# Performance work log

Hardware: AMD Instinct MI355X
Metric: run time of the kernel (lower is better)

The kernel has to match this reference:

```python
import jax, jax.numpy as jnp
import numpy as np

EMB = 2048
HEADS = 16


def setup_inputs() -> dict:
    key = jax.random.key(0)
    k_x, k_wqkv, k_bqkv, k_wo, k_bo = jax.random.split(key, 5)
    B, S, E = 2, 2048, EMB
    x = jax.random.normal(k_x, (B, S, E), dtype=jnp.float32)
    # nn.Linear weights stored as (in, out) for x @ W + b convention
    W_qkv = jax.random.normal(k_wqkv, (E, 3 * E), dtype=jnp.float32) * 0.02
    b_qkv = jax.random.normal(k_bqkv, (3 * E,), dtype=jnp.float32) * 0.02
    W_out = jax.random.normal(k_wo, (E, E), dtype=jnp.float32) * 0.02
    b_out = jax.random.normal(k_bo, (E,), dtype=jnp.float32) * 0.02
    return {"x": x, "W_qkv": W_qkv, "b_qkv": b_qkv, "W_out": W_out, "b_out": b_out}


def reference(x, W_qkv, b_qkv, W_out, b_out):
    B, S, E = x.shape
    H = HEADS
    dh = E // H
    # QKV projection: (B,S,3E)
    qkv = x @ W_qkv + b_qkv
    # Faithful to torch: reshape (B,S,H,3*dh) THEN split -> interleaved per-head q/k/v
    qkv = qkv.reshape(B, S, H, 3 * dh).transpose(0, 2, 1, 3)  # (B,H,S,3*dh)
    q, k, v = jnp.split(qkv, 3, axis=-1)  # each (B,H,S,dh)
    q = q / jnp.asarray(dh, q.dtype) ** 0.5
    scores = jnp.einsum('bhqd,bhkd->bhqk', q, k)  # (B,H,S,S)
    weights = jax.nn.softmax(scores, axis=-1)
    attn = jnp.einsum('bhqk,bhkd->bhqd', weights, v)  # (B,H,S,dh)
    attn = attn.transpose(0, 2, 1, 3).reshape(B, S, E)
    return attn @ W_out + b_out
```

## Files before the change

kernel.cpp:

```cpp
#include <hip/hip_runtime.h>
#include <type_traits>
#include <utility>

#define DI __device__ __forceinline__

typedef unsigned short u16;
typedef float f32x4 __attribute__((ext_vector_type(4)));
typedef float f32x16 __attribute__((ext_vector_type(16)));
typedef short s16x8 __attribute__((ext_vector_type(8)));
typedef __bf16 bf16x8 __attribute__((ext_vector_type(8)));

template <typename V, typename = void>
struct mfma_ok : std::false_type {};
template <typename V>
struct mfma_ok<V, std::void_t<decltype(__builtin_amdgcn_mfma_f32_16x16x32_bf16(
    std::declval<V>(), std::declval<V>(), std::declval<f32x4>(), 0, 0, 0))>>
    : std::true_type {};
using frag_t = std::conditional_t<mfma_ok<bf16x8>::value, bf16x8, s16x8>;

union U128 {
  int4 i;
  frag_t f;
  u16 s[8];
};

DI f32x4 mfma16(const U128& a, const U128& b, f32x4 c) {
  return __builtin_amdgcn_mfma_f32_16x16x32_bf16(a.f, b.f, c, 0, 0, 0);
}
DI f32x16 mfma32(const U128& a, const U128& b, f32x16 c) {
  return __builtin_amdgcn_mfma_f32_32x32x16_bf16(a.f, b.f, c, 0, 0, 0);
}

DI u16 f2b(float x) {
  union { float f; unsigned u; } v; v.f = x;
  unsigned r = v.u + 0x7FFFu + ((v.u >> 16) & 1u);
  return (u16)(r >> 16);
}

DI unsigned pk2bf(float a, float b) {
  unsigned short ua = __builtin_bit_cast(unsigned short, (__bf16)a);
  unsigned short ub = __builtin_bit_cast(unsigned short, (__bf16)b);
  return (unsigned)ua | ((unsigned)ub << 16);
}

#if __has_builtin(__builtin_amdgcn_exp2f)
#define EXP2F __builtin_amdgcn_exp2f
#else
#define EXP2F exp2f
#endif

DI void plswap(unsigned& lo, unsigned& hi) {
  asm("v_permlane32_swap_b32 %0, %1" : "+v"(lo), "+v"(hi));
}

typedef __attribute__((address_space(1))) void gas_t;
typedef __attribute__((address_space(3))) void las_t;
DI void gll16(const void* g, void* l) {
  __builtin_amdgcn_global_load_lds((gas_t*)g, (las_t*)l, 16, 0, 0);
}

#define QSCALE 0.12751791437603762f

__global__ __launch_bounds__(256) void k_conv_bf16(const float* __restrict__ in,
                                                   u16* __restrict__ out, int n4) {
  int i = blockIdx.x * 256 + threadIdx.x;
  if (i >= n4) return;
  float4 v = ((const float4*)in)[i];
  ushort4 o;
  o.x = f2b(v.x); o.y = f2b(v.y); o.z = f2b(v.z); o.w = f2b(v.w);
  ((ushort4*)out)[i] = o;
}

__global__ __launch_bounds__(256) void k_transpose_f2b(const float* __restrict__ in,
                                                       u16* __restrict__ out,
                                                       int R, int C) {
  __shared__ __attribute__((aligned(16))) u16 Tb[64][68];
  int t = threadIdx.x;
  long r0 = (long)blockIdx.y * 64, c0 = (long)blockIdx.x * 64;
  int cq = (t & 15) * 4, rr = t >> 4;
#pragma unroll
  for (int it = 0; it < 4; ++it) {
    int r = rr + it * 16;
    float4 v = *(const float4*)(in + (r0 + r) * C + c0 + cq);
    Tb[r][cq + 0] = f2b(v.x); Tb[r][cq + 1] = f2b(v.y);
    Tb[r][cq + 2] = f2b(v.z); Tb[r][cq + 3] = f2b(v.w);
  }
  __syncthreads();
#pragma unroll
  for (int it = 0; it < 2; ++it) {
    int ci = it * 256 + t;
    int cc = ci >> 3, ch = ci & 7, rb = ch * 8;
    unsigned p0 = Tb[rb + 0][cc] | ((unsigned)Tb[rb + 1][cc] << 16);
    unsigned p1 = Tb[rb + 2][cc] | ((unsigned)Tb[rb + 3][cc] << 16);
    unsigned p2 = Tb[rb + 4][cc] | ((unsigned)Tb[rb + 5][cc] << 16);
    unsigned p3 = Tb[rb + 6][cc] | ((unsigned)Tb[rb + 7][cc] << 16);
    *(int4*)(out + (c0 + cc) * R + r0 + rb) = make_int4(p0, p1, p2, p3);
  }
}

template <int MODE>
__global__ __launch_bounds__(256, 4) void k_gemm_bt(const u16* __restrict__ A,
                                                    const u16* __restrict__ Bt,
                                                    const float* __restrict__ bias,
                                                    void* __restrict__ Cout,
                                                    u16* __restrict__ qb,
                                                    u16* __restrict__ kbv,
                                                    u16* __restrict__ vb,
                                                    int n_off,
                                                    int M, int N, int K) {
  __shared__ __attribute__((aligned(16))) u16 As[128 * 64];
  __shared__ __attribute__((aligned(16))) u16 Bs[128 * 64];
  int t = threadIdx.x;
  int lane = t & 63, w = t >> 6, quad = lane >> 4, l15 = lane & 15;
  long m0 = (long)blockIdx.y * 128, n0 = n_off + (long)blockIdx.x * 128;
  int wr = (w >> 1) * 64, wc = (w & 1) * 64;
  int sw = l15 & 7;
  f32x4 acc[4][4] = {};
  for (int k0 = 0; k0 < K; k0 += 64) {
    __syncthreads();
#pragma unroll
    for (int it = 0; it < 4; ++it) {
      int ci = it * 256 + t;
      int row = ci >> 3, cl = (ci & 7) ^ (row & 7);
      gll16(A + (m0 + row) * K + k0 + cl * 8, As + ci * 8);
      gll16(Bt + (n0 + row) * K + k0 + cl * 8, Bs + ci * 8);
    }
    __syncthreads();
#pragma unroll
    for (int kk = 0; kk < 2; ++kk) {
      U128 a[4], b[4];
#pragma unroll
      for (int i = 0; i < 4; ++i)
        a[i].i = *(const int4*)(As + (wr + i * 16 + l15) * 64 + (((kk * 4 + quad) ^ sw) << 3));
#pragma unroll
      for (int j = 0; j < 4; ++j)
        b[j].i = *(const int4*)(Bs + (wc + j * 16 + l15) * 64 + (((kk * 4 + quad) ^ sw) << 3));
#pragma unroll
      for (int i = 0; i < 4; ++i)
#pragma unroll
        for (int j = 0; j < 4; ++j)
          acc[i][j] = mfma16(a[i], b[j], acc[i][j]);
    }
  }
  float bj[4];
#pragma unroll
  for (int j = 0; j < 4; ++j) bj[j] = bias[n0 + wc + j * 16 + l15];

  int hidx = (int)(n0 / 384);
  int rsel = (int)(n0 - hidx * 384) >> 7;
  u16* route = (MODE == 1) ? (rsel == 0 ? qb : rsel == 1 ? kbv : vb) : nullptr;

#pragma unroll
  for (int i = 0; i < 4; ++i) {
#pragma unroll
    for (int rr2 = 0; rr2 < 4; ++rr2) {
      long row = m0 + wr + i * 16 + quad * 4 + rr2;
#pragma unroll
      for (int j = 0; j < 4; ++j) {
        float v = acc[i][j][rr2] + bj[j];
        if (MODE == 1) {
          if (rsel == 0) v *= QSCALE;
          int bidx = (int)(row >> 11), s = (int)(row & 2047);
          long obase = ((long)(bidx * 16 + hidx) * 2048 + s) * 128;
          int dh = wc + j * 16 + l15;
          unsigned pb = f2b(v);
          unsigned other = __shfl_xor(pb, 1);
          if (!(l15 & 1))
            ((unsigned*)route)[(obase + dh) >> 1] = pb | (other << 16);
        } else {
          long col = n0 + wc + j * 16 + l15;
          unsigned bits = __float_as_uint(v);
          unsigned other = __shfl_xor(bits, 1);
          if (!(l15 & 1)) {
            uint2 pr; pr.x = bits; pr.y = other;
            *(uint2*)((float*)Cout + row * N + col) = pr;
          }
        }
      }
    }
  }
}

__global__ __launch_bounds__(256) void k_extract_vt(const u16* __restrict__ vb,
                                                    u16* __restrict__ vt) {
  __shared__ __attribute__((aligned(16))) u16 Vb[64][136];
  int t = threadIdx.x;
  int s0 = blockIdx.x * 64;
  int bh = blockIdx.y;
  long inbase = ((long)bh * 2048 + s0) * 128;
#pragma unroll
  for (int it = 0; it < 4; ++it) {
    int ci = it * 256 + t;
    int s = ci >> 4, ch = ci & 15;
    int4 v = *(const int4*)(vb + inbase + s * 128 + ch * 8);
    *(int4*)(&Vb[s][ch * 8]) = v;
  }
  __syncthreads();
  long outbase = (long)bh * 128 * 2048 + s0;
#pragma unroll
  for (int it = 0; it < 4; ++it) {
    int ci = it * 256 + t;
    int d = ci >> 3, ch = ci & 7, sb = ch * 8;
    unsigned p0 = Vb[sb + 0][d] | ((unsigned)Vb[sb + 1][d] << 16);
    unsigned p1 = Vb[sb + 2][d] | ((unsigned)Vb[sb + 3][d] << 16);
    unsigned p2 = Vb[sb + 4][d] | ((unsigned)Vb[sb + 5][d] << 16);
    unsigned p3 = Vb[sb + 6][d] | ((unsigned)Vb[sb + 7][d] << 16);
    *(int4*)(vt + outbase + (long)d * 2048 + sb) = make_int4(p0, p1, p2, p3);
  }
}

__global__ __launch_bounds__(256, 2) void k_flash(const u16* __restrict__ qb,
                                                  const u16* __restrict__ kb,
                                                  const u16* __restrict__ vt,
                                                  u16* __restrict__ attn) {
  __shared__ __attribute__((aligned(16))) u16 Ks[2][64 * 128];
  __shared__ __attribute__((aligned(16))) u16 Vts[2][128 * 64];
  int t = threadIdx.x;
  int lane = t & 63, w = t >> 6, l31 = lane & 31, h = lane >> 5;
  int q0 = blockIdx.x * 128 + w * 32;
  int bh = blockIdx.y, b = bh >> 4, hd = bh & 15;

  const u16* qbase = qb + ((long)bh * 2048 + q0 + l31) * 128;
  U128 qf[8];
#pragma unroll
  for (int dht = 0; dht < 8; ++dht)
    qf[dht].i = *(const int4*)(qbase + dht * 16 + h * 8);
  __syncthreads();

  f32x16 O[4] = {};
  float ls0 = 0.f, ls1 = 0.f, ls2 = 0.f, ls3 = 0.f;
  const u16* kbh = kb + (long)bh * 2048 * 128;
  long vbase = (long)bh * 128 * 2048;

  unsigned swx = (unsigned)(((l31 & 7) << 3) ^ (h << 3));
  unsigned kinv = ((unsigned)l31 << 7) ^ swx;
  unsigned vinv = ((unsigned)l31 << 6) ^ swx;

  auto stage = [&](int buf, int k0) {
#pragma unroll
    for (int it = 0; it < 4; ++it) {
      int ci = it * 256 + t;
      int key = ci >> 4, cp = ci & 15, cl = cp ^ (key & 7);
      gll16(kbh + (long)(k0 + key) * 128 + cl * 8, &Ks[buf][0] + ci * 8);
    }
#pragma unroll
    for (int it = 0; it < 4; ++it) {
      int ci = it * 256 + t;
      int d = ci >> 3, cp = ci & 7, cl = cp ^ (d & 7);
      gll16(vt + vbase + (long)d * 2048 + k0 + cl * 8, &Vts[buf][0] + ci * 8);
    }
  };

  stage(0, 0);
  int cur = 0;
  for (int k0 = 0; k0 < 2048; k0 += 64) {
    if (k0 + 64 < 2048) {
      stage(cur ^ 1, k0 + 64);
      asm volatile("s_waitcnt vmcnt(8)" ::: "memory");
    } else {
      asm volatile("s_waitcnt vmcnt(0)" ::: "memory");
    }
    __builtin_amdgcn_s_barrier();
    asm volatile("" ::: "memory");
    const u16* KbT = &Ks[cur][0];
    const u16* VbT = &Vts[cur][0];

    f32x16 St0 = {}, St1 = {};
    __builtin_amdgcn_s_setprio(1);
#pragma unroll
    for (int dht = 0; dht < 8; ++dht) {
      U128 kf;
      kf.i = *(const int4*)(KbT + (kinv ^ (unsigned)(dht << 4)));
      St0 = mfma32(kf, qf[dht], St0);
    }
#pragma unroll
    for (int dht = 0; dht < 8; ++dht) {
      U128 kf;
      kf.i = *(const int4*)(KbT + (kinv ^ (unsigned)(dht << 4)) + 4096);
      St1 = mfma32(kf, qf[dht], St1);
    }
    __builtin_amdgcn_s_setprio(0);

    auto pv = [&](int kt, const U128& pfk) {
#pragma unroll
      for (int dht = 0; dht < 4; ++dht) {
        U128 vf;
        vf.i = *(const int4*)(VbT + (vinv ^ (unsigned)(kt << 4)) + dht * 2048);
        O[dht] = mfma32(vf, pfk, O[dht]);
      }
    };
    auto mkpf = [&](const float* p) {
      unsigned w0 = pk2bf(p[0], p[1]);
      unsigned w1 = pk2bf(p[2], p[3]);
      unsigned w2 = pk2bf(p[4], p[5]);
      unsigned w3 = pk2bf(p[6], p[7]);
      plswap(w0, w2);
      plswap(w1, w3);
      U128 r; r.i = make_int4(w0, w1, w2, w3);
      return r;
    };

    float p0[16];
#pragma unroll
    for (int r = 0; r < 16; r += 4) {
      p0[r + 0] = EXP2F(St0[r + 0]); ls0 += p0[r + 0];
      p0[r + 1] = EXP2F(St0[r + 1]); ls1 += p0[r + 1];
      p0[r + 2] = EXP2F(St0[r + 2]); ls2 += p0[r + 2];
      p0[r + 3] = EXP2F(St0[r + 3]); ls3 += p0[r + 3];
    }
    U128 pf0 = mkpf(&p0[0]);
    U128 pf1 = mkpf(&p0[8]);

    pv(0, pf0);

    float p1[16];
#pragma unroll
    for (int r = 0; r < 8; r += 4) {
      p1[r + 0] = EXP2F(St1[r + 0]); ls0 += p1[r + 0];
      p1[r + 1] = EXP2F(St1[r + 1]); ls1 += p1[r + 1];
      p1[r + 2] = EXP2F(St1[r + 2]); ls2 += p1[r + 2];
      p1[r + 3] = EXP2F(St1[r + 3]); ls3 += p1[r + 3];
    }
    pv(1, pf1);

#pragma unroll
    for (int r = 8; r < 16; r += 4) {
      p1[r + 0] = EXP2F(St1[r + 0]); ls0 += p1[r + 0];
      p1[r + 1] = EXP2F(St1[r + 1]); ls1 += p1[r + 1];
      p1[r + 2] = EXP2F(St1[r + 2]); ls2 += p1[r + 2];
      p1[r + 3] = EXP2F(St1[r + 3]); ls3 += p1[r + 3];
    }
    U128 pf2 = mkpf(&p1[0]);
    U128 pf3 = mkpf(&p1[8]);

    __builtin_amdgcn_s_setprio(1);
    pv(2, pf2);
    pv(3, pf3);
    __builtin_amdgcn_s_setprio(0);

    asm volatile("" ::: "memory");
    __builtin_amdgcn_s_barrier();
    cur ^= 1;
  }

  float lsum = (ls0 + ls1) + (ls2 + ls3);
  float ltot = lsum + __shfl_xor(lsum, 32);
  float inv = 1.f / ltot;
  long orow = (long)b * 2048 + q0 + l31;
  u16* ob = attn + orow * 2048 + hd * 128;
#pragma unroll
  for (int dht = 0; dht < 4; ++dht)
#pragma unroll
    for (int g = 0; g < 4; ++g) {
      int dh = dht * 32 + g * 8 + h * 4;
      float v0 = O[dht][4 * g + 0] * inv, v1 = O[dht][4 * g + 1] * inv;
      float v2 = O[dht][4 * g + 2] * inv, v3 = O[dht][4 * g + 3] * inv;
      uint2 pkd;
      pkd.x = pk2bf(v0, v1);
      pkd.y = pk2bf(v2, v3);
      *(uint2*)(ob + dh) = pkd;
    }
}

extern "C" void kernel_launch(void* const* d_in, const int* in_sizes, int n_in,
                              void* d_out, int out_size, void* d_ws, size_t ws_size,
                              hipStream_t stream) {
  const float* x    = (const float*)d_in[0];
  const float* Wqkv = (const float*)d_in[1];
  const float* bqkv = (const float*)d_in[2];
  const float* Wout = (const float*)d_in[3];
  const float* bout = (const float*)d_in[4];
  float* out = (float*)d_out;
  char* ws = (char*)d_ws;

  if (ws_size < 75497472u) return;

  u16* xb    = (u16*)d_out;
  u16* wqkvt = (u16*)(ws);
  u16* qbuf  = (u16*)(ws + 25165824);
  u16* kbuf  = (u16*)(ws + 41943040);
  u16* vbuf  = (u16*)(ws + 58720256);
  u16* vtb   = (u16*)d_out;
  u16* woutt = (u16*)(ws);
  u16* attnb = (u16*)(ws + 8388608);

  k_conv_bf16<<<8192, 256, 0, stream>>>(x, xb, 2097152);
  k_transpose_f2b<<<dim3(96, 32), 256, 0, stream>>>(Wqkv, wqkvt, 2048, 6144);
  k_gemm_bt<1><<<dim3(48, 32), 256, 0, stream>>>(xb, wqkvt, bqkv, nullptr,
                                                 qbuf, kbuf, vbuf, 0, 4096, 6144, 2048);
  k_extract_vt<<<dim3(32, 32), 256, 0, stream>>>(vbuf, vtb);
  k_transpose_f2b<<<dim3(32, 32), 256, 0, stream>>>(Wout, woutt, 2048, 2048);
  k_flash<<<dim3(16, 32), 256, 0, stream>>>(qbuf, kbuf, vtb, attnb);
  k_gemm_bt<0><<<dim3(16, 32), 256, 0, stream>>>(attnb, woutt, bout, out,
                                                 nullptr, nullptr, nullptr, 0, 4096, 2048, 2048);
}
```

Measured before the change: 383.3 us.

## Fuse V transpose into QKV GEMM epilogue and merge small prep kernels

The QKV GEMM epilogue for V tiles now stages the tile in shared memory and writes V directly in transposed layout, which removes the separate extract_vt kernel and its round trip of V through memory. The x conversion and Wqkv transpose are merged into one launch, and the Wout transpose blocks are appended to the flash-attention grid. Together these cut the launch count from seven to four and drop one intermediate buffer pass. The cost is a shared-memory epilogue with extra syncs in the GEMM, and the flash grid now mixes tiles of very different work.

Result: faster. 364.8 us (-4.8%).

```diff
diff --git a/kernel.cpp b/kernel.cpp
--- a/kernel.cpp
+++ b/kernel.cpp
@@ -61,22 +61,9 @@
 
 #define QSCALE 0.12751791437603762f
 
-__global__ __launch_bounds__(256) void k_conv_bf16(const float* __restrict__ in,
-                                                   u16* __restrict__ out, int n4) {
-  int i = blockIdx.x * 256 + threadIdx.x;
-  if (i >= n4) return;
-  float4 v = ((const float4*)in)[i];
-  ushort4 o;
-  o.x = f2b(v.x); o.y = f2b(v.y); o.z = f2b(v.z); o.w = f2b(v.w);
-  ((ushort4*)out)[i] = o;
-}
-
-__global__ __launch_bounds__(256) void k_transpose_f2b(const float* __restrict__ in,
-                                                       u16* __restrict__ out,
-                                                       int R, int C) {
-  __shared__ __attribute__((aligned(16))) u16 Tb[64][68];
-  int t = threadIdx.x;
-  long r0 = (long)blockIdx.y * 64, c0 = (long)blockIdx.x * 64;
+DI void transpose_tile(const float* __restrict__ in, u16* __restrict__ out,
+                       int R, int C, int bx, int by, int t, u16 (*Tb)[68]) {
+  long r0 = (long)by * 64, c0 = (long)bx * 64;
   int cq = (t & 15) * 4, rr = t >> 4;
 #pragma unroll
   for (int it = 0; it < 4; ++it) {
@@ -98,6 +85,24 @@
   }
 }
 
+__global__ __launch_bounds__(256) void k_pre(const float* __restrict__ x,
+                                             u16* __restrict__ xb,
+                                             const float* __restrict__ Wqkv,
+                                             u16* __restrict__ wqkvt) {
+  __shared__ __attribute__((aligned(16))) u16 Tb[64][68];
+  int bid = blockIdx.x, t = threadIdx.x;
+  if (bid < 8192) {
+    int i = bid * 256 + t;
+    float4 v = ((const float4*)x)[i];
+    ushort4 o;
+    o.x = f2b(v.x); o.y = f2b(v.y); o.z = f2b(v.z); o.w = f2b(v.w);
+    ((ushort4*)xb)[i] = o;
+    return;
+  }
+  int idx = bid - 8192;
+  transpose_tile(Wqkv, wqkvt, 2048, 6144, idx % 96, idx / 96, t, Tb);
+}
+
 template <int MODE>
 __global__ __launch_bounds__(256, 4) void k_gemm_bt(const u16* __restrict__ A,
                                                     const u16* __restrict__ Bt,
@@ -105,11 +110,12 @@
                                                     void* __restrict__ Cout,
                                                     u16* __restrict__ qb,
                                                     u16* __restrict__ kbv,
-                                                    u16* __restrict__ vb,
+                                                    u16* __restrict__ vt,
                                                     int n_off,
                                                     int M, int N, int K) {
-  __shared__ __attribute__((aligned(16))) u16 As[128 * 64];
-  __shared__ __attribute__((aligned(16))) u16 Bs[128 * 64];
+  __shared__ __attribute__((aligned(16))) u16 SM[16384];
+  u16* As = SM;
+  u16* Bs = SM + 8192;
   int t = threadIdx.x;
   int lane = t & 63, w = t >> 6, quad = lane >> 4, l15 = lane & 15;
   long m0 = (long)blockIdx.y * 128, n0 = n_off + (long)blockIdx.x * 128;
@@ -148,7 +154,35 @@
 
   int hidx = (int)(n0 / 384);
   int rsel = (int)(n0 - hidx * 384) >> 7;
-  u16* route = (MODE == 1) ? (rsel == 0 ? qb : rsel == 1 ? kbv : vb) : nullptr;
+
+  if (MODE == 1 && rsel == 2) {
+    __syncthreads();
+#pragma unroll
+    for (int i = 0; i < 4; ++i)
+#pragma unroll
+      for (int rr2 = 0; rr2 < 4; ++rr2) {
+        int m = wr + i * 16 + quad * 4 + rr2;
+#pragma unroll
+        for (int j = 0; j < 4; ++j)
+          SM[m * 128 + wc + j * 16 + l15] = f2b(acc[i][j][rr2] + bj[j]);
+      }
+    __syncthreads();
+    int bidx = (int)(m0 >> 11), s0 = (int)(m0 & 2047);
+    u16* vrow = vt + (long)(bidx * 16 + hidx) * 128 * 2048 + s0;
+#pragma unroll
+    for (int it = 0; it < 8; ++it) {
+      int ci = it * 256 + t;
+      int d = ci & 127, sb = (ci >> 7) * 8;
+      unsigned p0 = SM[(sb + 0) * 128 + d] | ((unsigned)SM[(sb + 1) * 128 + d] << 16);
+      unsigned p1 = SM[(sb + 2) * 128 + d] | ((unsigned)SM[(sb + 3) * 128 + d] << 16);
+      unsigned p2 = SM[(sb + 4) * 128 + d] | ((unsigned)SM[(sb + 5) * 128 + d] << 16);
+      unsigned p3 = SM[(sb + 6) * 128 + d] | ((unsigned)SM[(sb + 7) * 128 + d] << 16);
+      *(int4*)(vrow + (long)d * 2048 + sb) = make_int4(p0, p1, p2, p3);
+    }
+    return;
+  }
+
+  u16* route = (MODE == 1) ? (rsel == 0 ? qb : kbv) : nullptr;
 
 #pragma unroll
   for (int i = 0; i < 4; ++i) {
@@ -181,40 +215,20 @@
   }
 }
 
-__global__ __launch_bounds__(256) void k_extract_vt(const u16* __restrict__ vb,
-                                                    u16* __restrict__ vt) {
-  __shared__ __attribute__((aligned(16))) u16 Vb[64][136];
-  int t = threadIdx.x;
-  int s0 = blockIdx.x * 64;
-  int bh = blockIdx.y;
-  long inbase = ((long)bh * 2048 + s0) * 128;
-#pragma unroll
-  for (int it = 0; it < 4; ++it) {
-    int ci = it * 256 + t;
-    int s = ci >> 4, ch = ci & 15;
-    int4 v = *(const int4*)(vb + inbase + s * 128 + ch * 8);
-    *(int4*)(&Vb[s][ch * 8]) = v;
-  }
-  __syncthreads();
-  long outbase = (long)bh * 128 * 2048 + s0;
-#pragma unroll
-  for (int it = 0; it < 4; ++it) {
-    int ci = it * 256 + t;
-    int d = ci >> 3, ch = ci & 7, sb = ch * 8;
-    unsigned p0 = Vb[sb + 0][d] | ((unsigned)Vb[sb + 1][d] << 16);
-    unsigned p1 = Vb[sb + 2][d] | ((unsigned)Vb[sb + 3][d] << 16);
-    unsigned p2 = Vb[sb + 4][d] | ((unsigned)Vb[sb + 5][d] << 16);
-    unsigned p3 = Vb[sb + 6][d] | ((unsigned)Vb[sb + 7][d] << 16);
-    *(int4*)(vt + outbase + (long)d * 2048 + sb) = make_int4(p0, p1, p2, p3);
-  }
-}
-
 __global__ __launch_bounds__(256, 2) void k_flash(const u16* __restrict__ qb,
                                                   const u16* __restrict__ kb,
                                                   const u16* __restrict__ vt,
-                                                  u16* __restrict__ attn) {
+                                                  u16* __restrict__ attn,
+                                                  const float* __restrict__ Wout,
+                                                  u16* __restrict__ woutt) {
   __shared__ __attribute__((aligned(16))) u16 Ks[2][64 * 128];
   __shared__ __attribute__((aligned(16))) u16 Vts[2][128 * 64];
+  if (blockIdx.y >= 32) {
+    u16 (*Tb)[68] = (u16(*)[68])(&Ks[0][0]);
+    int u = (blockIdx.y - 32) * 16 + blockIdx.x;
+    transpose_tile(Wout, woutt, 2048, 2048, u & 31, u >> 5, threadIdx.x, Tb);
+    return;
+  }
   int t = threadIdx.x;
   int lane = t & 63, w = t >> 6, l31 = lane & 31, h = lane >> 5;
   int q0 = blockIdx.x * 128 + w * 32;
@@ -379,18 +393,14 @@
   u16* wqkvt = (u16*)(ws);
   u16* qbuf  = (u16*)(ws + 25165824);
   u16* kbuf  = (u16*)(ws + 41943040);
-  u16* vbuf  = (u16*)(ws + 58720256);
-  u16* vtb   = (u16*)d_out;
+  u16* vtb   = (u16*)(ws + 58720256);
   u16* woutt = (u16*)(ws);
   u16* attnb = (u16*)(ws + 8388608);
 
-  k_conv_bf16<<<8192, 256, 0, stream>>>(x, xb, 2097152);
-  k_transpose_f2b<<<dim3(96, 32), 256, 0, stream>>>(Wqkv, wqkvt, 2048, 6144);
+  k_pre<<<11264, 256, 0, stream>>>(x, xb, Wqkv, wqkvt);
   k_gemm_bt<1><<<dim3(48, 32), 256, 0, stream>>>(xb, wqkvt, bqkv, nullptr,
-                                                 qbuf, kbuf, vbuf, 0, 4096, 6144, 2048);
-  k_extract_vt<<<dim3(32, 32), 256, 0, stream>>>(vbuf, vtb);
-  k_transpose_f2b<<<dim3(32, 32), 256, 0, stream>>>(Wout, woutt, 2048, 2048);
-  k_flash<<<dim3(16, 32), 256, 0, stream>>>(qbuf, kbuf, vtb, attnb);
+                                                 qbuf, kbuf, vtb, 0, 4096, 6144, 2048);
+  k_flash<<<dim3(16, 96), 256, 0, stream>>>(qbuf, kbuf, vtb, attnb, Wout, woutt);
   k_gemm_bt<0><<<dim3(16, 32), 256, 0, stream>>>(attnb, woutt, bout, out,
                                                  nullptr, nullptr, nullptr, 0, 4096, 2048, 2048);
 }
```
